# Kernel optimization log

Measured on AMD Instinct MI355X. Metric: run time of the kernel, lower is better.

The kernel has to match this reference:

```python
import jax, jax.numpy as jnp
import numpy as np

F = 64          # in_feature == out_feature
H = 64          # hidden_feature
L = 2           # hidden_layer
B = 32768       # batch


def celu(x):
    # CELU with alpha=1.0: max(0,x) + min(0, exp(x)-1)
    return jnp.where(x > 0, x, jnp.expm1(x))


def setup_inputs() -> dict:
    key = jax.random.key(0)
    ks = jax.random.split(key, 7)
    s_in = 1.0                      # fan_in=1 for first layer
    s_h = 1.0 / np.sqrt(H)
    return {
        "x": jax.random.normal(ks[0], (B, F), dtype=jnp.float32),
        # Linear(1, H) per feature: weight [F, H], bias [F, H]
        "w_in": jax.random.uniform(ks[1], (F, H), jnp.float32, -s_in, s_in),
        "b_in": jax.random.uniform(ks[2], (F, H), jnp.float32, -s_in, s_in),
        # hidden Linear(H, H) per feature per layer: weight [L, F, H(out), H(in)]
        "w_hid": jax.random.uniform(ks[3], (L, F, H, H), jnp.float32, -s_h, s_h),
        "b_hid": jax.random.uniform(ks[4], (L, F, H), jnp.float32, -s_h, s_h),
        # Linear(H, 1) per feature: weight [F, H], bias [F]
        "w_out": jax.random.uniform(ks[5], (F, H), jnp.float32, -s_h, s_h),
        "b_out": jax.random.uniform(ks[6], (F,), jnp.float32, -s_h, s_h),
    }


def reference(x, w_in, b_in, w_hid, b_hid, w_out, b_out):
    # x: [B, F] -> per-feature scalar input to F independent MLPs
    # First layer: Linear(1, H) per feature, then CELU
    h = celu(x[:, :, None] * w_in[None, :, :] + b_in[None, :, :])   # [B, F, H]
    # Hidden layers (small fixed count L) -- batched GEMM over F
    for l in range(L):
        # torch Linear: y = h @ W^T + b, W is [out, in] -> einsum over in-axis
        h = celu(jnp.einsum('bfh,fkh->bfk', h, w_hid[l]) + b_hid[l][None, :, :])
    # Output layer: Linear(H, 1) per feature, concatenated along feature dim
    out = jnp.einsum('bfh,fh->bf', h, w_out) + b_out[None, :]       # [B, F]
    return out
```

## Files before the change

kernel.cpp:

```cpp
#include <hip/hip_runtime.h>

#define F 64
#define H 64
#define NT 256
#define TILE_ROWS 128
#define ITERS 8
#define ROWS_PER_BLOCK (TILE_ROWS * ITERS)
#define WPAD 72

typedef __bf16 bf16;
typedef __attribute__((ext_vector_type(8))) __bf16 bf16x8;
typedef __attribute__((ext_vector_type(4))) __bf16 bf16x4;
typedef __attribute__((ext_vector_type(4))) float f32x4;

__device__ __forceinline__ float celu1(float v) {
    float e = __expf(v) - 1.0f;
    return v > 0.0f ? v : e;
}

__global__ __launch_bounds__(256) void prep(const float* __restrict__ w, bf16* __restrict__ wc,
                                            const float* __restrict__ x, float* __restrict__ xT,
                                            int R) {
    const int t = threadIdx.x;
    __shared__ float tile[64][65];
    if (blockIdx.x < 512) {
        int i = (blockIdx.x * 256 + t) * 4;
        float4 v = *(const float4*)(w + i);
        bf16x4 o; o[0] = (bf16)v.x; o[1] = (bf16)v.y; o[2] = (bf16)v.z; o[3] = (bf16)v.w;
        *(bf16x4*)(wc + i) = o;
        return;
    }
    const int r0 = (int)(blockIdx.x - 512) * 64;
    {
        const int c4 = t & 15, rr = t >> 4;
        #pragma unroll
        for (int i = 0; i < 4; ++i) {
            float4 v = *(const float4*)(x + (size_t)(r0 + rr + i * 16) * 64 + c4 * 4);
            tile[rr + i * 16][c4 * 4 + 0] = v.x;
            tile[rr + i * 16][c4 * 4 + 1] = v.y;
            tile[rr + i * 16][c4 * 4 + 2] = v.z;
            tile[rr + i * 16][c4 * 4 + 3] = v.w;
        }
    }
    __syncthreads();
    {
        const int b4 = t & 15, f0 = t >> 4;
        #pragma unroll
        for (int i = 0; i < 4; ++i) {
            int ff = f0 + i * 16;
            float4 v;
            v.x = tile[b4 * 4 + 0][ff];
            v.y = tile[b4 * 4 + 1][ff];
            v.z = tile[b4 * 4 + 2][ff];
            v.w = tile[b4 * 4 + 3][ff];
            *(float4*)(xT + (size_t)ff * R + r0 + b4 * 4) = v;
        }
    }
}

__global__ __launch_bounds__(256) void transpose_bwd(const float* __restrict__ src,
                                                     float* __restrict__ dst, int R) {
    __shared__ float tile[64][65];
    const int t = threadIdx.x;
    const int r0 = blockIdx.x * 64;
    {
        const int b4 = t & 15, f0 = t >> 4;
        #pragma unroll
        for (int i = 0; i < 4; ++i) {
            int ff = f0 + i * 16;
            float4 v = *(const float4*)(src + (size_t)ff * R + r0 + b4 * 4);
            tile[b4 * 4 + 0][ff] = v.x;
            tile[b4 * 4 + 1][ff] = v.y;
            tile[b4 * 4 + 2][ff] = v.z;
            tile[b4 * 4 + 3][ff] = v.w;
        }
    }
    __syncthreads();
    {
        const int c4 = t & 15, rr = t >> 4;
        #pragma unroll
        for (int i = 0; i < 4; ++i) {
            float4 v;
            v.x = tile[rr + i * 16][c4 * 4 + 0];
            v.y = tile[rr + i * 16][c4 * 4 + 1];
            v.z = tile[rr + i * 16][c4 * 4 + 2];
            v.w = tile[rr + i * 16][c4 * 4 + 3];
            *(float4*)(dst + (size_t)(r0 + rr + i * 16) * 64 + c4 * 4) = v;
        }
    }
}

template<bool PLANA>
__global__ __launch_bounds__(NT, 3) void mlp64(
    const float* __restrict__ x,
    const float* __restrict__ xT,
    int Btot,
    const float* __restrict__ w_in,
    const float* __restrict__ b_in,
    const float* __restrict__ w_hid,
    const float* __restrict__ b_hid,
    const float* __restrict__ w_out,
    const float* __restrict__ b_out,
    const bf16*  __restrict__ wc,
    float* __restrict__ out,
    float* __restrict__ outT)
{
    const int f    = blockIdx.x & (F - 1);
    const int blk  = blockIdx.x >> 6;
    const int row0 = blk * ROWS_PER_BLOCK;
    const int t    = threadIdx.x;
    const int lane = t & 63;
    const int wave = t >> 6;
    const int l15  = lane & 15;
    const int q    = lane >> 4;
    const int wrow = wave * 32;

    __shared__ __align__(16) bf16 hbuf[TILE_ROWS][WPAD];
    __shared__ __align__(16) bf16 wlds[H][WPAD];
    __shared__ __align__(16) float s_bias[3][H];

    for (int idx = t; idx < 512; idx += NT) {
        const int row = idx >> 3, ch = idx & 7;
        if (PLANA) {
            bf16x8 v = *(const bf16x8*)(wc + (((size_t)F + f) << 12) + (row << 6) + (ch << 3));
            *(bf16x8*)&wlds[row][ch * 8] = v;
        } else {
            const float* p = w_hid + (((size_t)F + f) << 12) + (row << 6) + (ch << 3);
            float4 a = *(const float4*)p, b = *(const float4*)(p + 4);
            bf16x8 v;
            v[0] = (bf16)a.x; v[1] = (bf16)a.y; v[2] = (bf16)a.z; v[3] = (bf16)a.w;
            v[4] = (bf16)b.x; v[5] = (bf16)b.y; v[6] = (bf16)b.z; v[7] = (bf16)b.w;
            *(bf16x8*)&wlds[row][ch * 8] = v;
        }
    }
    if (t < H)           s_bias[0][t]         = b_in[f * H + t];
    else if (t < 2 * H)  s_bias[1][t - H]     = b_hid[(0 * F + f) * H + (t - H)];
    else if (t < 3 * H)  s_bias[2][t - 2 * H] = b_hid[(1 * F + f) * H + (t - 2 * H)];
    __syncthreads();

    bf16x8 Aw0[4][2];
    #pragma unroll
    for (int m = 0; m < 4; ++m) {
        if (PLANA) {
            const bf16* p = wc + ((size_t)f << 12) + (m * 16 + l15) * 64 + q * 8;
            Aw0[m][0] = *(const bf16x8*)p;
            Aw0[m][1] = *(const bf16x8*)(p + 32);
        } else {
            const float* p = w_hid + ((size_t)f << 12) + (m * 16 + l15) * 64 + q * 8;
            #pragma unroll
            for (int kk = 0; kk < 2; ++kk) {
                float4 a = *(const float4*)(p + kk * 32), b = *(const float4*)(p + kk * 32 + 4);
                bf16x8 v;
                v[0] = (bf16)a.x; v[1] = (bf16)a.y; v[2] = (bf16)a.z; v[3] = (bf16)a.w;
                v[4] = (bf16)b.x; v[5] = (bf16)b.y; v[6] = (bf16)b.z; v[7] = (bf16)b.w;
                Aw0[m][kk] = v;
            }
        }
    }

    bf16x8 A1[4];
    #pragma unroll
    for (int m = 0; m < 4; ++m) {
        float w  = w_in[f * H + m * 16 + l15];
        bf16 hi  = (bf16)w;
        bf16 lo  = (bf16)(w - (float)hi);
        bf16x8 v = {};
        if (q == 0) { v[0] = hi; v[1] = lo; v[2] = hi; }
        A1[m] = v;
    }

    f32x4 wo4[4];
    #pragma unroll
    for (int m = 0; m < 4; ++m)
        wo4[m] = *(const f32x4*)(w_out + f * H + m * 16 + q * 4);
    const float bo = b_out[f];

    const float* xcol = PLANA ? (xT + (size_t)f * Btot) : nullptr;
    float*       ocol = PLANA ? (outT + (size_t)f * Btot) : nullptr;

    float xc0, xc1;
    if (PLANA) {
        xc0 = xcol[row0 + wrow + l15];
        xc1 = xcol[row0 + wrow + 16 + l15];
    } else {
        xc0 = x[(size_t)(row0 + wrow + l15) * F + f];
        xc1 = x[(size_t)(row0 + wrow + 16 + l15) * F + f];
    }

    #pragma unroll 1
    for (int it = 0; it < ITERS; ++it) {
        const int rbase = row0 + it * TILE_ROWS + wrow;

        bf16x8 B1[2];
        {
            bf16 h0 = (bf16)xc0, h1 = (bf16)xc1;
            bf16 l0 = (bf16)(xc0 - (float)h0), l1 = (bf16)(xc1 - (float)h1);
            bf16x8 v0 = {}, v1 = {};
            if (q == 0) { v0[0] = h0; v0[1] = h0; v0[2] = l0;
                          v1[0] = h1; v1[1] = h1; v1[2] = l1; }
            B1[0] = v0; B1[1] = v1;
        }
        float xn0 = 0.0f, xn1 = 0.0f;
        if (it + 1 < ITERS) {
            if (PLANA) {
                xn0 = xcol[rbase + TILE_ROWS + l15];
                xn1 = xcol[rbase + TILE_ROWS + 16 + l15];
            } else {
                xn0 = x[(size_t)(rbase + TILE_ROWS + l15) * F + f];
                xn1 = x[(size_t)(rbase + TILE_ROWS + 16 + l15) * F + f];
            }
        }

        #pragma unroll
        for (int m = 0; m < 4; ++m) {
            f32x4 c0 = *(const f32x4*)&s_bias[0][m * 16 + q * 4];
            f32x4 a0 = __builtin_amdgcn_mfma_f32_16x16x32_bf16(A1[m], B1[0], c0, 0, 0, 0);
            f32x4 a1 = __builtin_amdgcn_mfma_f32_16x16x32_bf16(A1[m], B1[1], c0, 0, 0, 0);
            bf16x4 o0, o1;
            #pragma unroll
            for (int rr = 0; rr < 4; ++rr) { o0[rr] = (bf16)celu1(a0[rr]); o1[rr] = (bf16)celu1(a1[rr]); }
            *(bf16x4*)&hbuf[wrow + l15][m * 16 + q * 4]      = o0;
            *(bf16x4*)&hbuf[wrow + 16 + l15][m * 16 + q * 4] = o1;
        }

        {
            bf16x8 Bh[2][2];
            #pragma unroll
            for (int n = 0; n < 2; ++n)
                #pragma unroll
                for (int kk = 0; kk < 2; ++kk)
                    Bh[n][kk] = *(const bf16x8*)&hbuf[wrow + n * 16 + l15][kk * 32 + q * 8];
            #pragma unroll
            for (int m = 0; m < 4; ++m) {
                f32x4 c0 = *(const f32x4*)&s_bias[1][m * 16 + q * 4];
                f32x4 a0 = __builtin_amdgcn_mfma_f32_16x16x32_bf16(Aw0[m][0], Bh[0][0], c0, 0, 0, 0);
                a0       = __builtin_amdgcn_mfma_f32_16x16x32_bf16(Aw0[m][1], Bh[0][1], a0, 0, 0, 0);
                f32x4 a1 = __builtin_amdgcn_mfma_f32_16x16x32_bf16(Aw0[m][0], Bh[1][0], c0, 0, 0, 0);
                a1       = __builtin_amdgcn_mfma_f32_16x16x32_bf16(Aw0[m][1], Bh[1][1], a1, 0, 0, 0);
                bf16x4 o0, o1;
                #pragma unroll
                for (int rr = 0; rr < 4; ++rr) { o0[rr] = (bf16)celu1(a0[rr]); o1[rr] = (bf16)celu1(a1[rr]); }
                *(bf16x4*)&hbuf[wrow + l15][m * 16 + q * 4]      = o0;
                *(bf16x4*)&hbuf[wrow + 16 + l15][m * 16 + q * 4] = o1;
            }
        }

        {
            bf16x8 Bh[2][2];
            #pragma unroll
            for (int n = 0; n < 2; ++n)
                #pragma unroll
                for (int kk = 0; kk < 2; ++kk)
                    Bh[n][kk] = *(const bf16x8*)&hbuf[wrow + n * 16 + l15][kk * 32 + q * 8];
            float s0 = 0.0f, s1 = 0.0f;
            #pragma unroll
            for (int m = 0; m < 4; ++m) {
                bf16x8 Awt0 = *(const bf16x8*)&wlds[m * 16 + l15][q * 8];
                bf16x8 Awt1 = *(const bf16x8*)&wlds[m * 16 + l15][32 + q * 8];
                f32x4 c0 = *(const f32x4*)&s_bias[2][m * 16 + q * 4];
                f32x4 a0 = __builtin_amdgcn_mfma_f32_16x16x32_bf16(Awt0, Bh[0][0], c0, 0, 0, 0);
                a0       = __builtin_amdgcn_mfma_f32_16x16x32_bf16(Awt1, Bh[0][1], a0, 0, 0, 0);
                f32x4 a1 = __builtin_amdgcn_mfma_f32_16x16x32_bf16(Awt0, Bh[1][0], c0, 0, 0, 0);
                a1       = __builtin_amdgcn_mfma_f32_16x16x32_bf16(Awt1, Bh[1][1], a1, 0, 0, 0);
                #pragma unroll
                for (int rr = 0; rr < 4; ++rr) {
                    s0 = fmaf(celu1(a0[rr]), wo4[m][rr], s0);
                    s1 = fmaf(celu1(a1[rr]), wo4[m][rr], s1);
                }
            }
            s0 += __shfl_xor(s0, 16, 64);
            s0 += __shfl_xor(s0, 32, 64);
            s1 += __shfl_xor(s1, 16, 64);
            s1 += __shfl_xor(s1, 32, 64);
            if (q == 0) {
                if (PLANA) {
                    ocol[rbase + l15]      = s0 + bo;
                    ocol[rbase + 16 + l15] = s1 + bo;
                } else {
                    out[(size_t)(rbase + l15) * F + f]      = s0 + bo;
                    out[(size_t)(rbase + 16 + l15) * F + f] = s1 + bo;
                }
            }
        }

        xc0 = xn0; xc1 = xn1;
    }
}

extern "C" void kernel_launch(void* const* d_in, const int* in_sizes, int n_in,
                              void* d_out, int out_size, void* d_ws, size_t ws_size,
                              hipStream_t stream) {
    const float* x     = (const float*)d_in[0];
    const float* w_in  = (const float*)d_in[1];
    const float* b_in  = (const float*)d_in[2];
    const float* w_hid = (const float*)d_in[3];
    const float* b_hid = (const float*)d_in[4];
    const float* w_out = (const float*)d_in[5];
    const float* b_out = (const float*)d_in[6];
    float* out = (float*)d_out;

    const int Btot = in_sizes[0] / F;
    dim3 grid((unsigned)((Btot / ROWS_PER_BLOCK) * F));
    dim3 block(NT);

    const int wn = 2 * F * H * H;
    const size_t wc_bytes = (size_t)wn * sizeof(bf16);
    const size_t xT_bytes = (size_t)Btot * F * sizeof(float);
    const size_t need = wc_bytes + 2 * xT_bytes;

    if (ws_size >= need) {
        bf16*  wcp  = (bf16*)d_ws;
        float* xT   = (float*)((char*)d_ws + wc_bytes);
        float* outT = (float*)((char*)d_ws + wc_bytes + xT_bytes);
        prep<<<512 + Btot / 64, 256, 0, stream>>>(w_hid, wcp, x, xT, Btot);
        mlp64<true><<<grid, block, 0, stream>>>(x, xT, Btot, w_in, b_in, w_hid, b_hid,
                                                w_out, b_out, wcp, out, outT);
        transpose_bwd<<<Btot / 64, 256, 0, stream>>>(outT, out, Btot);
    } else {
        mlp64<false><<<grid, block, 0, stream>>>(x, nullptr, Btot, w_in, b_in, w_hid, b_hid,
                                                 w_out, b_out, nullptr, out, nullptr);
    }
}
```

Baseline: 182.0 us.

## Drop prep and transpose kernels, run single fused MLP kernel reading x directly

Removes the weight-to-bf16 prep kernel and the x/out transpose kernels, so the MLP kernel reads row-major x with a stride of F and converts the fp32 hidden weights to bf16 in-kernel. This saves two extra launches and the workspace round trips. It also raises the launch-bounds occupancy hint from 3 to 4 blocks per CU. The cost is strided, uncoalesced 4-byte reads and writes of x and out per feature column, and repeated fp32 weight loads with conversion in every block.

```diff
diff --git a/kernel.cpp b/kernel.cpp
--- a/kernel.cpp
+++ b/kernel.cpp
@@ -18,92 +18,16 @@
     return v > 0.0f ? v : e;
 }
 
-__global__ __launch_bounds__(256) void prep(const float* __restrict__ w, bf16* __restrict__ wc,
-                                            const float* __restrict__ x, float* __restrict__ xT,
-                                            int R) {
-    const int t = threadIdx.x;
-    __shared__ float tile[64][65];
-    if (blockIdx.x < 512) {
-        int i = (blockIdx.x * 256 + t) * 4;
-        float4 v = *(const float4*)(w + i);
-        bf16x4 o; o[0] = (bf16)v.x; o[1] = (bf16)v.y; o[2] = (bf16)v.z; o[3] = (bf16)v.w;
-        *(bf16x4*)(wc + i) = o;
-        return;
-    }
-    const int r0 = (int)(blockIdx.x - 512) * 64;
-    {
-        const int c4 = t & 15, rr = t >> 4;
-        #pragma unroll
-        for (int i = 0; i < 4; ++i) {
-            float4 v = *(const float4*)(x + (size_t)(r0 + rr + i * 16) * 64 + c4 * 4);
-            tile[rr + i * 16][c4 * 4 + 0] = v.x;
-            tile[rr + i * 16][c4 * 4 + 1] = v.y;
-            tile[rr + i * 16][c4 * 4 + 2] = v.z;
-            tile[rr + i * 16][c4 * 4 + 3] = v.w;
-        }
-    }
-    __syncthreads();
-    {
-        const int b4 = t & 15, f0 = t >> 4;
-        #pragma unroll
-        for (int i = 0; i < 4; ++i) {
-            int ff = f0 + i * 16;
-            float4 v;
-            v.x = tile[b4 * 4 + 0][ff];
-            v.y = tile[b4 * 4 + 1][ff];
-            v.z = tile[b4 * 4 + 2][ff];
-            v.w = tile[b4 * 4 + 3][ff];
-            *(float4*)(xT + (size_t)ff * R + r0 + b4 * 4) = v;
-        }
-    }
-}
-
-__global__ __launch_bounds__(256) void transpose_bwd(const float* __restrict__ src,
-                                                     float* __restrict__ dst, int R) {
-    __shared__ float tile[64][65];
-    const int t = threadIdx.x;
-    const int r0 = blockIdx.x * 64;
-    {
-        const int b4 = t & 15, f0 = t >> 4;
-        #pragma unroll
-        for (int i = 0; i < 4; ++i) {
-            int ff = f0 + i * 16;
-            float4 v = *(const float4*)(src + (size_t)ff * R + r0 + b4 * 4);
-            tile[b4 * 4 + 0][ff] = v.x;
-            tile[b4 * 4 + 1][ff] = v.y;
-            tile[b4 * 4 + 2][ff] = v.z;
-            tile[b4 * 4 + 3][ff] = v.w;
-        }
-    }
-    __syncthreads();
-    {
-        const int c4 = t & 15, rr = t >> 4;
-        #pragma unroll
-        for (int i = 0; i < 4; ++i) {
-            float4 v;
-            v.x = tile[rr + i * 16][c4 * 4 + 0];
-            v.y = tile[rr + i * 16][c4 * 4 + 1];
-            v.z = tile[rr + i * 16][c4 * 4 + 2];
-            v.w = tile[rr + i * 16][c4 * 4 + 3];
-            *(float4*)(dst + (size_t)(r0 + rr + i * 16) * 64 + c4 * 4) = v;
-        }
-    }
-}
-
-template<bool PLANA>
-__global__ __launch_bounds__(NT, 3) void mlp64(
+__global__ __launch_bounds__(NT, 4) void mlp64(
     const float* __restrict__ x,
-    const float* __restrict__ xT,
-    int Btot,
     const float* __restrict__ w_in,
     const float* __restrict__ b_in,
     const float* __restrict__ w_hid,
     const float* __restrict__ b_hid,
     const float* __restrict__ w_out,
     const float* __restrict__ b_out,
-    const bf16*  __restrict__ wc,
     float* __restrict__ out,
-    float* __restrict__ outT)
+    int Btot)
 {
     const int f    = blockIdx.x & (F - 1);
     const int blk  = blockIdx.x >> 6;
@@ -121,17 +45,12 @@
 
     for (int idx = t; idx < 512; idx += NT) {
         const int row = idx >> 3, ch = idx & 7;
-        if (PLANA) {
-            bf16x8 v = *(const bf16x8*)(wc + (((size_t)F + f) << 12) + (row << 6) + (ch << 3));
-            *(bf16x8*)&wlds[row][ch * 8] = v;
-        } else {
-            const float* p = w_hid + (((size_t)F + f) << 12) + (row << 6) + (ch << 3);
-            float4 a = *(const float4*)p, b = *(const float4*)(p + 4);
-            bf16x8 v;
-            v[0] = (bf16)a.x; v[1] = (bf16)a.y; v[2] = (bf16)a.z; v[3] = (bf16)a.w;
-            v[4] = (bf16)b.x; v[5] = (bf16)b.y; v[6] = (bf16)b.z; v[7] = (bf16)b.w;
-            *(bf16x8*)&wlds[row][ch * 8] = v;
-        }
+        const float* p = w_hid + (((size_t)F + f) << 12) + (row << 6) + (ch << 3);
+        float4 a = *(const float4*)p, b = *(const float4*)(p + 4);
+        bf16x8 v;
+        v[0] = (bf16)a.x; v[1] = (bf16)a.y; v[2] = (bf16)a.z; v[3] = (bf16)a.w;
+        v[4] = (bf16)b.x; v[5] = (bf16)b.y; v[6] = (bf16)b.z; v[7] = (bf16)b.w;
+        *(bf16x8*)&wlds[row][ch * 8] = v;
     }
     if (t < H)           s_bias[0][t]         = b_in[f * H + t];
     else if (t < 2 * H)  s_bias[1][t - H]     = b_hid[(0 * F + f) * H + (t - H)];
@@ -141,20 +60,14 @@
     bf16x8 Aw0[4][2];
     #pragma unroll
     for (int m = 0; m < 4; ++m) {
-        if (PLANA) {
-            const bf16* p = wc + ((size_t)f << 12) + (m * 16 + l15) * 64 + q * 8;
-            Aw0[m][0] = *(const bf16x8*)p;
-            Aw0[m][1] = *(const bf16x8*)(p + 32);
-        } else {
-            const float* p = w_hid + ((size_t)f << 12) + (m * 16 + l15) * 64 + q * 8;
-            #pragma unroll
-            for (int kk = 0; kk < 2; ++kk) {
-                float4 a = *(const float4*)(p + kk * 32), b = *(const float4*)(p + kk * 32 + 4);
-                bf16x8 v;
-                v[0] = (bf16)a.x; v[1] = (bf16)a.y; v[2] = (bf16)a.z; v[3] = (bf16)a.w;
-                v[4] = (bf16)b.x; v[5] = (bf16)b.y; v[6] = (bf16)b.z; v[7] = (bf16)b.w;
-                Aw0[m][kk] = v;
-            }
+        const float* p = w_hid + ((size_t)f << 12) + (m * 16 + l15) * 64 + q * 8;
+        #pragma unroll
+        for (int kk = 0; kk < 2; ++kk) {
+            float4 a = *(const float4*)(p + kk * 32), b = *(const float4*)(p + kk * 32 + 4);
+            bf16x8 v;
+            v[0] = (bf16)a.x; v[1] = (bf16)a.y; v[2] = (bf16)a.z; v[3] = (bf16)a.w;
+            v[4] = (bf16)b.x; v[5] = (bf16)b.y; v[6] = (bf16)b.z; v[7] = (bf16)b.w;
+            Aw0[m][kk] = v;
         }
     }
 
@@ -175,17 +88,8 @@
         wo4[m] = *(const f32x4*)(w_out + f * H + m * 16 + q * 4);
     const float bo = b_out[f];
 
-    const float* xcol = PLANA ? (xT + (size_t)f * Btot) : nullptr;
-    float*       ocol = PLANA ? (outT + (size_t)f * Btot) : nullptr;
-
-    float xc0, xc1;
-    if (PLANA) {
-        xc0 = xcol[row0 + wrow + l15];
-        xc1 = xcol[row0 + wrow + 16 + l15];
-    } else {
-        xc0 = x[(size_t)(row0 + wrow + l15) * F + f];
-        xc1 = x[(size_t)(row0 + wrow + 16 + l15) * F + f];
-    }
+    float xc0 = x[(size_t)(row0 + wrow + l15) * F + f];
+    float xc1 = x[(size_t)(row0 + wrow + 16 + l15) * F + f];
 
     #pragma unroll 1
     for (int it = 0; it < ITERS; ++it) {
@@ -202,13 +106,8 @@
         }
         float xn0 = 0.0f, xn1 = 0.0f;
         if (it + 1 < ITERS) {
-            if (PLANA) {
-                xn0 = xcol[rbase + TILE_ROWS + l15];
-                xn1 = xcol[rbase + TILE_ROWS + 16 + l15];
-            } else {
-                xn0 = x[(size_t)(rbase + TILE_ROWS + l15) * F + f];
-                xn1 = x[(size_t)(rbase + TILE_ROWS + 16 + l15) * F + f];
-            }
+            xn0 = x[(size_t)(rbase + TILE_ROWS + l15) * F + f];
+            xn1 = x[(size_t)(rbase + TILE_ROWS + 16 + l15) * F + f];
         }
 
         #pragma unroll
@@ -273,13 +172,8 @@
             s1 += __shfl_xor(s1, 16, 64);
             s1 += __shfl_xor(s1, 32, 64);
             if (q == 0) {
-                if (PLANA) {
-                    ocol[rbase + l15]      = s0 + bo;
-                    ocol[rbase + 16 + l15] = s1 + bo;
-                } else {
-                    out[(size_t)(rbase + l15) * F + f]      = s0 + bo;
-                    out[(size_t)(rbase + 16 + l15) * F + f] = s1 + bo;
-                }
+                out[(size_t)(rbase + l15) * F + f]      = s0 + bo;
+                out[(size_t)(rbase + 16 + l15) * F + f] = s1 + bo;
             }
         }
 
@@ -302,22 +196,5 @@
     const int Btot = in_sizes[0] / F;
     dim3 grid((unsigned)((Btot / ROWS_PER_BLOCK) * F));
     dim3 block(NT);
-
-    const int wn = 2 * F * H * H;
-    const size_t wc_bytes = (size_t)wn * sizeof(bf16);
-    const size_t xT_bytes = (size_t)Btot * F * sizeof(float);
-    const size_t need = wc_bytes + 2 * xT_bytes;
-
-    if (ws_size >= need) {
-        bf16*  wcp  = (bf16*)d_ws;
-        float* xT   = (float*)((char*)d_ws + wc_bytes);
-        float* outT = (float*)((char*)d_ws + wc_bytes + xT_bytes);
-        prep<<<512 + Btot / 64, 256, 0, stream>>>(w_hid, wcp, x, xT, Btot);
-        mlp64<true><<<grid, block, 0, stream>>>(x, xT, Btot, w_in, b_in, w_hid, b_hid,
-                                                w_out, b_out, wcp, out, outT);
-        transpose_bwd<<<Btot / 64, 256, 0, stream>>>(outT, out, Btot);
-    } else {
-        mlp64<false><<<grid, block, 0, stream>>>(x, nullptr, Btot, w_in, b_in, w_hid, b_hid,
-                                                 w_out, b_out, nullptr, out, nullptr);
-    }
+    mlp64<<<grid, block, 0, stream>>>(x, w_in, b_in, w_hid, b_hid, w_out, b_out, out, Btot);
 }
```

Result: slower. 287.4 us (+58.0%).
